# Optimization experiments

Measured on AMD Instinct MI355X. Metric: run time of the kernel, lower is better.

The kernel has to match this reference:

```python
import jax, jax.numpy as jnp
import numpy as np

B, I, H = 65536, 256, 256

def setup_inputs() -> dict:
    key = jax.random.key(0)
    ks = jax.random.split(key, 7)
    stdv = 1.0 / np.sqrt(H)
    u = lambda k, shape: jax.random.uniform(k, shape, jnp.float32, -stdv, stdv)
    return {
        "x":  jax.random.normal(ks[0], (B, I), jnp.float32),
        "h":  jax.random.normal(ks[1], (B, H), jnp.float32),
        "c":  jax.random.normal(ks[2], (B, H), jnp.float32),
        "Wi": u(ks[3], (4, H, I)),   # stacked [W_ii, W_if, W_ig, W_io], torch layout [out,in]
        "Wh": u(ks[4], (4, H, H)),   # stacked [W_hi, W_hf, W_hg, W_ho]
        "bi": u(ks[5], (4, H)),
        "bh": u(ks[6], (4, H)),
    }

def reference(x, h, c, Wi, Wh, bi, bh):
    # Fused version of 8 separate Linears: two batched GEMMs + one elementwise pass.
    # gates[b, k, h] = x @ Wi[k].T + h_prev @ Wh[k].T + bi[k] + bh[k]
    gates = (jnp.einsum('bi,khi->bkh', x, Wi)
             + jnp.einsum('bj,khj->bkh', h, Wh)
             + bi[None] + bh[None])
    i = jax.nn.sigmoid(gates[:, 0])
    f = jax.nn.sigmoid(gates[:, 1])
    g = jnp.tanh(gates[:, 2])
    o = jax.nn.sigmoid(gates[:, 3])
    c_new = f * c + i * g
    h_new = o * jnp.tanh(c_new)
    return (h_new, c_new)
```

## Files before the change

### kernel.cpp

```cpp
#include <hip/hip_runtime.h>
#include <stdint.h>

#define B_DIM 65536
#define HOFF  16777216

typedef __attribute__((ext_vector_type(8))) short short8;
typedef __attribute__((ext_vector_type(8))) unsigned short ushort8_t;
typedef __attribute__((ext_vector_type(4))) float f32x4;

__device__ __forceinline__ unsigned short f2bf(float f) {
  unsigned int u = __builtin_bit_cast(unsigned int, f);
  u += 0x7FFFu + ((u >> 16) & 1u);
  return (unsigned short)(u >> 16);
}
__device__ __forceinline__ float sigf(float x) { return 1.0f / (1.0f + __expf(-x)); }
__device__ __forceinline__ float tanh_fast(float x) {
  float a = fabsf(x);
  float e = __expf(-2.0f * a);
  float t = (1.0f - e) / (1.0f + e);
  return x < 0.0f ? -t : t;
}

typedef const __attribute__((address_space(1))) unsigned int* as1p;
typedef __attribute__((address_space(3))) unsigned int* as3p;
__device__ __forceinline__ void llds16(const unsigned short* g, unsigned short* l) {
  __builtin_amdgcn_global_load_lds((as1p)g, (as3p)l, 16, 0, 0);
}

__global__ void prep_a(const float* __restrict__ x, const float* __restrict__ h,
                       ushort8_t* __restrict__ A8) {
  unsigned o = blockIdx.x * 256u + threadIdx.x;
  unsigned b = o >> 6, c8 = o & 63u;
  const float* src = (c8 < 32u) ? x + (size_t)b * 256u + c8 * 8u
                                : h + (size_t)b * 256u + (c8 - 32u) * 8u;
  float4 v0 = *(const float4*)src;
  float4 v1 = *(const float4*)(src + 4);
  ushort8_t p;
  p[0] = f2bf(v0.x); p[1] = f2bf(v0.y); p[2] = f2bf(v0.z); p[3] = f2bf(v0.w);
  p[4] = f2bf(v1.x); p[5] = f2bf(v1.y); p[6] = f2bf(v1.z); p[7] = f2bf(v1.w);
  A8[o] = p;
}

__global__ void prep_w(const float* __restrict__ Wi, const float* __restrict__ Wh,
                       ushort8_t* __restrict__ W8) {
  unsigned o = blockIdx.x * 256u + threadIdx.x;
  unsigned n = o >> 6, c8 = o & 63u;
  const float* src = (c8 < 32u) ? Wi + (size_t)n * 256u + c8 * 8u
                                : Wh + (size_t)n * 256u + (c8 - 32u) * 8u;
  float4 v0 = *(const float4*)src;
  float4 v1 = *(const float4*)(src + 4);
  ushort8_t p;
  p[0] = f2bf(v0.x); p[1] = f2bf(v0.y); p[2] = f2bf(v0.z); p[3] = f2bf(v0.w);
  p[4] = f2bf(v1.x); p[5] = f2bf(v1.y); p[6] = f2bf(v1.z); p[7] = f2bf(v1.w);
  W8[o] = p;
}

__global__ __launch_bounds__(256, 4) void lstm_gemm(
    const unsigned short* __restrict__ A,
    const unsigned short* __restrict__ W,
    const float* __restrict__ cprev,
    const float* __restrict__ bi, const float* __restrict__ bh,
    float* __restrict__ out) {
  __shared__ unsigned short sA[128 * 32];
  __shared__ unsigned short sB[128 * 32];

  const int t = threadIdx.x;
  const int wid = t >> 6, lane = t & 63;
  const int m = lane & 15, q = lane >> 4;
  const int b0 = (int)(blockIdx.x >> 3) * 128;
  const int h0 = (int)(blockIdx.x & 7) * 32;
  const int R = (wid >> 1) * 64, Cc = (wid & 1) * 64;
  const int hcol = h0 + ((Cc >> 6) << 4) + m;

  const int l4 = lane >> 2;
  const int sg0 = wid * 2, sg1 = wid * 2 + 1;
  const int r0 = sg0 * 16 + l4, r1 = sg1 * 16 + l4;
  const int ck = ((lane & 3) ^ ((l4 >> 1) & 3)) * 8;
  const unsigned aO0 = (unsigned)(b0 + r0) * 512u + (unsigned)ck;
  const unsigned aO1 = (unsigned)(b0 + r1) * 512u + (unsigned)ck;
  const int n0 = (((r0 >> 4) & 3) << 8) + h0 + (r0 & 15) + ((r0 >> 6) << 4);
  const int n1 = (((r1 >> 4) & 3) << 8) + h0 + (r1 & 15) + ((r1 >> 6) << 4);
  const unsigned wO0 = (unsigned)n0 * 512u + (unsigned)ck;
  const unsigned wO1 = (unsigned)n1 * 512u + (unsigned)ck;
  unsigned short* dA0 = &sA[sg0 * 512];
  unsigned short* dA1 = &sA[sg1 * 512];
  unsigned short* dB0 = &sB[sg0 * 512];
  unsigned short* dB1 = &sB[sg1 * 512];

  const int swz = (q ^ ((m >> 1) & 3)) * 8;

  f32x4 acc[4][4];
#pragma unroll
  for (int j = 0; j < 4; ++j) {
    float bv = bi[(j << 8) + hcol] + bh[(j << 8) + hcol];
    f32x4 z = {bv, bv, bv, bv};
#pragma unroll
    for (int i = 0; i < 4; ++i) acc[i][j] = z;
  }

  for (int kt = 0; kt < 16; ++kt) {
    const unsigned k0 = kt * 32u;
    llds16(A + aO0 + k0, dA0);
    llds16(A + aO1 + k0, dA1);
    llds16(W + wO0 + k0, dB0);
    llds16(W + wO1 + k0, dB1);
    __syncthreads();
    short8 av[4], bv[4];
#pragma unroll
    for (int i = 0; i < 4; ++i)
      av[i] = *(const short8*)&sA[(R + i * 16 + m) * 32 + swz];
#pragma unroll
    for (int j = 0; j < 4; ++j)
      bv[j] = *(const short8*)&sB[(Cc + j * 16 + m) * 32 + swz];
#pragma unroll
    for (int i = 0; i < 4; ++i)
#pragma unroll
      for (int j = 0; j < 4; ++j)
        acc[i][j] = __builtin_amdgcn_mfma_f32_16x16x32_bf16(av[i], bv[j], acc[i][j], 0, 0, 0);
    __syncthreads();
  }

  const float* cp = cprev + hcol;
  float* oh = out + hcol;
  float* oc = out + HOFF + hcol;
#pragma unroll
  for (int i = 0; i < 4; ++i) {
    const int br = b0 + R + i * 16 + (q << 2);
    float cv[4];
#pragma unroll
    for (int r = 0; r < 4; ++r) cv[r] = cp[(size_t)(br + r) << 8];
#pragma unroll
    for (int r = 0; r < 4; ++r) {
      float iv = sigf(acc[i][0][r]);
      float fv = sigf(acc[i][1][r]);
      float gv = tanh_fast(acc[i][2][r]);
      float ov = sigf(acc[i][3][r]);
      float cn = fv * cv[r] + iv * gv;
      oh[(size_t)(br + r) << 8] = ov * tanh_fast(cn);
      oc[(size_t)(br + r) << 8] = cn;
    }
  }
}

__global__ void lstm_naive(const float* __restrict__ x, const float* __restrict__ h,
                           const float* __restrict__ c,
                           const float* __restrict__ Wi, const float* __restrict__ Wh,
                           const float* __restrict__ bi, const float* __restrict__ bh,
                           float* __restrict__ out) {
  int gid = blockIdx.x * 256 + threadIdx.x;
  int b = gid >> 8, hh = gid & 255;
  float a0 = bi[hh] + bh[hh];
  float a1 = bi[256 + hh] + bh[256 + hh];
  float a2 = bi[512 + hh] + bh[512 + hh];
  float a3 = bi[768 + hh] + bh[768 + hh];
  const float* xr = x + (size_t)b * 256;
  const float* hr = h + (size_t)b * 256;
  const float* w0 = Wi + (size_t)hh * 256;
  const float* w1 = Wh + (size_t)hh * 256;
  for (int i = 0; i < 256; ++i) {
    float xv = xr[i];
    a0 += xv * w0[i]; a1 += xv * w0[65536 + i];
    a2 += xv * w0[131072 + i]; a3 += xv * w0[196608 + i];
  }
  for (int i = 0; i < 256; ++i) {
    float hv = hr[i];
    a0 += hv * w1[i]; a1 += hv * w1[65536 + i];
    a2 += hv * w1[131072 + i]; a3 += hv * w1[196608 + i];
  }
  float iv = sigf(a0), fv = sigf(a1), gv = tanh_fast(a2), ov = sigf(a3);
  float cn = fv * c[gid] + iv * gv;
  out[gid] = ov * tanh_fast(cn);
  out[HOFF + gid] = cn;
}

extern "C" void kernel_launch(void* const* d_in, const int* in_sizes, int n_in,
                              void* d_out, int out_size, void* d_ws, size_t ws_size,
                              hipStream_t stream) {
  const float* x  = (const float*)d_in[0];
  const float* h  = (const float*)d_in[1];
  const float* c  = (const float*)d_in[2];
  const float* Wi = (const float*)d_in[3];
  const float* Wh = (const float*)d_in[4];
  const float* bi = (const float*)d_in[5];
  const float* bh = (const float*)d_in[6];
  float* out = (float*)d_out;

  const size_t needA = (size_t)B_DIM * 512 * 2;
  const size_t needW = (size_t)1024 * 512 * 2;
  if (ws_size >= needA + needW) {
    ushort8_t* A8 = (ushort8_t*)d_ws;
    ushort8_t* W8 = (ushort8_t*)((char*)d_ws + needA);
    hipLaunchKernelGGL(prep_a, dim3(B_DIM * 64 / 256), dim3(256), 0, stream, x, h, A8);
    hipLaunchKernelGGL(prep_w, dim3(1024 * 64 / 256), dim3(256), 0, stream, Wi, Wh, W8);
    hipLaunchKernelGGL(lstm_gemm, dim3((B_DIM / 128) * 8), dim3(256), 0, stream,
                       (const unsigned short*)A8, (const unsigned short*)W8,
                       c, bi, bh, out);
  } else {
    hipLaunchKernelGGL(lstm_naive, dim3(B_DIM), dim3(256), 0, stream,
                       x, h, c, Wi, Wh, bi, bh, out);
  }
}
```

Baseline: 417.3 us.

## Fuse activation bf16 conversion into GEMM with pipelined loads and LDS-staged epilogue

Result: slower. 448.7 us (+7.5%).

```diff
diff --git a/kernel.cpp b/kernel.cpp
--- a/kernel.cpp
+++ b/kernel.cpp
@@ -8,11 +8,16 @@
 typedef __attribute__((ext_vector_type(8))) unsigned short ushort8_t;
 typedef __attribute__((ext_vector_type(4))) float f32x4;
 
-__device__ __forceinline__ unsigned short f2bf(float f) {
-  unsigned int u = __builtin_bit_cast(unsigned int, f);
+__device__ __forceinline__ unsigned f2bf_u(float f) {
+  unsigned u = __builtin_bit_cast(unsigned, f);
   u += 0x7FFFu + ((u >> 16) & 1u);
-  return (unsigned short)(u >> 16);
-}
+  return u >> 16;
+}
+__device__ __forceinline__ unsigned pack2(float lo, float hi) {
+  return f2bf_u(lo) | (f2bf_u(hi) << 16);
+}
+__device__ __forceinline__ unsigned short f2bf(float f) { return (unsigned short)f2bf_u(f); }
+
 __device__ __forceinline__ float sigf(float x) { return 1.0f / (1.0f + __expf(-x)); }
 __device__ __forceinline__ float tanh_fast(float x) {
   float a = fabsf(x);
@@ -27,19 +32,8 @@
   __builtin_amdgcn_global_load_lds((as1p)g, (as3p)l, 16, 0, 0);
 }
 
-__global__ void prep_a(const float* __restrict__ x, const float* __restrict__ h,
-                       ushort8_t* __restrict__ A8) {
-  unsigned o = blockIdx.x * 256u + threadIdx.x;
-  unsigned b = o >> 6, c8 = o & 63u;
-  const float* src = (c8 < 32u) ? x + (size_t)b * 256u + c8 * 8u
-                                : h + (size_t)b * 256u + (c8 - 32u) * 8u;
-  float4 v0 = *(const float4*)src;
-  float4 v1 = *(const float4*)(src + 4);
-  ushort8_t p;
-  p[0] = f2bf(v0.x); p[1] = f2bf(v0.y); p[2] = f2bf(v0.z); p[3] = f2bf(v0.w);
-  p[4] = f2bf(v1.x); p[5] = f2bf(v1.y); p[6] = f2bf(v1.z); p[7] = f2bf(v1.w);
-  A8[o] = p;
-}
+#define SYNC_LGKM() asm volatile("s_waitcnt lgkmcnt(0)\n\ts_barrier" ::: "memory")
+#define WAVE_LDS_FENCE() asm volatile("s_waitcnt lgkmcnt(0)" ::: "memory")
 
 __global__ void prep_w(const float* __restrict__ Wi, const float* __restrict__ Wh,
                        ushort8_t* __restrict__ W8) {
@@ -55,90 +49,125 @@
   W8[o] = p;
 }
 
-__global__ __launch_bounds__(256, 4) void lstm_gemm(
-    const unsigned short* __restrict__ A,
+__global__ __launch_bounds__(256, 3) void lstm_fused(
+    const float* __restrict__ X, const float* __restrict__ Hs,
     const unsigned short* __restrict__ W,
     const float* __restrict__ cprev,
     const float* __restrict__ bi, const float* __restrict__ bh,
     float* __restrict__ out) {
-  __shared__ unsigned short sA[128 * 32];
-  __shared__ unsigned short sB[128 * 32];
+  __shared__ union {
+    struct { unsigned short A[128 * 32]; unsigned short B[2][128 * 32]; } s;
+    float ep[4 * 1152];
+  } sm;
 
   const int t = threadIdx.x;
   const int wid = t >> 6, lane = t & 63;
   const int m = lane & 15, q = lane >> 4;
   const int b0 = (int)(blockIdx.x >> 3) * 128;
   const int h0 = (int)(blockIdx.x & 7) * 32;
-  const int R = (wid >> 1) * 64, Cc = (wid & 1) * 64;
-  const int hcol = h0 + ((Cc >> 6) << 4) + m;
+  const int R = wid * 32;
 
   const int l4 = lane >> 2;
-  const int sg0 = wid * 2, sg1 = wid * 2 + 1;
-  const int r0 = sg0 * 16 + l4, r1 = sg1 * 16 + l4;
-  const int ck = ((lane & 3) ^ ((l4 >> 1) & 3)) * 8;
-  const unsigned aO0 = (unsigned)(b0 + r0) * 512u + (unsigned)ck;
-  const unsigned aO1 = (unsigned)(b0 + r1) * 512u + (unsigned)ck;
-  const int n0 = (((r0 >> 4) & 3) << 8) + h0 + (r0 & 15) + ((r0 >> 6) << 4);
-  const int n1 = (((r1 >> 4) & 3) << 8) + h0 + (r1 & 15) + ((r1 >> 6) << 4);
-  const unsigned wO0 = (unsigned)n0 * 512u + (unsigned)ck;
-  const unsigned wO1 = (unsigned)n1 * 512u + (unsigned)ck;
-  unsigned short* dA0 = &sA[sg0 * 512];
-  unsigned short* dA1 = &sA[sg1 * 512];
-  unsigned short* dB0 = &sB[sg0 * 512];
-  unsigned short* dB1 = &sB[sg1 * 512];
-
-  const int swz = (q ^ ((m >> 1) & 3)) * 8;
-
-  f32x4 acc[4][4];
-#pragma unroll
-  for (int j = 0; j < 4; ++j) {
-    float bv = bi[(j << 8) + hcol] + bh[(j << 8) + hcol];
-    f32x4 z = {bv, bv, bv, bv};
-#pragma unroll
-    for (int i = 0; i < 4; ++i) acc[i][j] = z;
-  }
-
+  const int sg0 = wid * 2, sg1 = sg0 + 1;
+  const int c0 = sg0 * 16 + l4, c1 = sg1 * 16 + l4;
+  const int ckb = ((lane & 3) ^ ((l4 >> 1) & 3)) * 8;
+  const int n0 = (((c0 >> 4) & 3) << 8) + h0 + (c0 & 15) + ((c0 >> 6) << 4);
+  const int n1 = (((c1 >> 4) & 3) << 8) + h0 + (c1 & 15) + ((c1 >> 6) << 4);
+  const unsigned wO0 = (unsigned)n0 * 512u + (unsigned)ckb;
+  const unsigned wO1 = (unsigned)n1 * 512u + (unsigned)ckb;
+
+  const int ar = t >> 1, hf = t & 1;
+  const unsigned aoff = (unsigned)(b0 + ar) * 256u + (unsigned)hf * 16u;
+  const int slot0 = (2 * hf) ^ ((ar >> 1) & 3), slot1 = slot0 ^ 1;
+  uint4* dA0 = (uint4*)&sm.s.A[ar * 32 + slot0 * 8];
+  uint4* dA1 = (uint4*)&sm.s.A[ar * 32 + slot1 * 8];
+
+  const int swzb = (q ^ ((m >> 1) & 3)) * 8;
+  const unsigned short* aRd = &sm.s.A[(R + m) * 32 + swzb];
+  const int bRdOff = m * 32 + swzb;
+
+  f32x4 acc[2][8];
+#pragma unroll
+  for (int jj = 0; jj < 8; ++jj) {
+    int g = jj & 3, hcol = h0 + ((jj >> 2) << 4) + m;
+    float bvv = bi[(g << 8) + hcol] + bh[(g << 8) + hcol];
+    f32x4 z = {bvv, bvv, bvv, bvv};
+    acc[0][jj] = z; acc[1][jj] = z;
+  }
+
+  float4 a0, a1, a2, a3;
+  { const float* p = X + aoff;
+    a0 = *(const float4*)p;       a1 = *(const float4*)(p + 4);
+    a2 = *(const float4*)(p + 8); a3 = *(const float4*)(p + 12); }
+  llds16(W + wO0, &sm.s.B[0][sg0 * 512]);
+  llds16(W + wO1, &sm.s.B[0][sg1 * 512]);
+
+#pragma unroll 2
   for (int kt = 0; kt < 16; ++kt) {
-    const unsigned k0 = kt * 32u;
-    llds16(A + aO0 + k0, dA0);
-    llds16(A + aO1 + k0, dA1);
-    llds16(W + wO0 + k0, dB0);
-    llds16(W + wO1 + k0, dB1);
+    const int cur = kt & 1, nxt = cur ^ 1;
+    uint4 u0, u1;
+    u0.x = pack2(a0.x, a0.y); u0.y = pack2(a0.z, a0.w);
+    u0.z = pack2(a1.x, a1.y); u0.w = pack2(a1.z, a1.w);
+    u1.x = pack2(a2.x, a2.y); u1.y = pack2(a2.z, a2.w);
+    u1.z = pack2(a3.x, a3.y); u1.w = pack2(a3.z, a3.w);
+    *dA0 = u0; *dA1 = u1;
     __syncthreads();
-    short8 av[4], bv[4];
-#pragma unroll
-    for (int i = 0; i < 4; ++i)
-      av[i] = *(const short8*)&sA[(R + i * 16 + m) * 32 + swz];
-#pragma unroll
-    for (int j = 0; j < 4; ++j)
-      bv[j] = *(const short8*)&sB[(Cc + j * 16 + m) * 32 + swz];
-#pragma unroll
-    for (int i = 0; i < 4; ++i)
-#pragma unroll
-      for (int j = 0; j < 4; ++j)
-        acc[i][j] = __builtin_amdgcn_mfma_f32_16x16x32_bf16(av[i], bv[j], acc[i][j], 0, 0, 0);
-    __syncthreads();
-  }
-
-  const float* cp = cprev + hcol;
-  float* oh = out + hcol;
-  float* oc = out + HOFF + hcol;
-#pragma unroll
-  for (int i = 0; i < 4; ++i) {
-    const int br = b0 + R + i * 16 + (q << 2);
-    float cv[4];
-#pragma unroll
-    for (int r = 0; r < 4; ++r) cv[r] = cp[(size_t)(br + r) << 8];
-#pragma unroll
-    for (int r = 0; r < 4; ++r) {
-      float iv = sigf(acc[i][0][r]);
-      float fv = sigf(acc[i][1][r]);
-      float gv = tanh_fast(acc[i][2][r]);
-      float ov = sigf(acc[i][3][r]);
-      float cn = fv * cv[r] + iv * gv;
-      oh[(size_t)(br + r) << 8] = ov * tanh_fast(cn);
-      oc[(size_t)(br + r) << 8] = cn;
+    if (kt < 15) {
+      llds16(W + wO0 + (unsigned)(kt + 1) * 32u, &sm.s.B[nxt][sg0 * 512]);
+      llds16(W + wO1 + (unsigned)(kt + 1) * 32u, &sm.s.B[nxt][sg1 * 512]);
     }
+    short8 av[2], bv[8];
+    av[0] = *(const short8*)aRd;
+    av[1] = *(const short8*)(aRd + 16 * 32);
+#pragma unroll
+    for (int jj = 0; jj < 8; ++jj)
+      bv[jj] = *(const short8*)&sm.s.B[cur][jj * 512 + bRdOff];
+    if (kt < 15) {
+      const float* src = ((kt + 1) < 8) ? X : Hs;
+      const float* p = src + aoff + ((unsigned)(kt + 1) & 7u) * 32u;
+      a0 = *(const float4*)p;       a1 = *(const float4*)(p + 4);
+      a2 = *(const float4*)(p + 8); a3 = *(const float4*)(p + 12);
+    }
+    SYNC_LGKM();
+#pragma unroll
+    for (int i = 0; i < 2; ++i)
+#pragma unroll
+      for (int jj = 0; jj < 8; ++jj)
+        acc[i][jj] = __builtin_amdgcn_mfma_f32_16x16x32_bf16(av[i], bv[jj], acc[i][jj], 0, 0, 0);
+  }
+
+  float* EB = sm.ep + wid * 1152;
+  const int ROWB = b0 + R;
+#pragma unroll
+  for (int i = 0; i < 2; ++i) {
+#pragma unroll
+    for (int ch = 0; ch < 2; ++ch)
+#pragma unroll
+      for (int r = 0; r < 4; ++r) {
+        int row = ROWB + i * 16 + q * 4 + r;
+        float cv = cprev[(size_t)row * 256 + h0 + ch * 16 + m];
+        float iv = sigf(acc[i][ch * 4 + 0][r]);
+        float fv = sigf(acc[i][ch * 4 + 1][r]);
+        float gv = tanh_fast(acc[i][ch * 4 + 2][r]);
+        float ov = sigf(acc[i][ch * 4 + 3][r]);
+        float cn = fv * cv + iv * gv;
+        float hn = ov * tanh_fast(cn);
+        int lrow = q * 4 + r, col = ch * 16 + m;
+        EB[lrow * 36 + col] = hn;
+        EB[576 + lrow * 36 + col] = cn;
+      }
+    WAVE_LDS_FENCE();
+    int lr = lane & 15, cb = (lane >> 4) * 8;
+    float4 hv0 = *(const float4*)&EB[lr * 36 + cb];
+    float4 hv1 = *(const float4*)&EB[lr * 36 + cb + 4];
+    float4 cv0 = *(const float4*)&EB[576 + lr * 36 + cb];
+    float4 cv1 = *(const float4*)&EB[576 + lr * 36 + cb + 4];
+    size_t gro = (size_t)(ROWB + i * 16 + lr) * 256 + h0 + cb;
+    *(float4*)&out[gro] = hv0;
+    *(float4*)&out[gro + 4] = hv1;
+    *(float4*)&out[HOFF + gro] = cv0;
+    *(float4*)&out[HOFF + gro + 4] = cv1;
+    if (i == 0) WAVE_LDS_FENCE();
   }
 }
 
@@ -185,16 +214,12 @@
   const float* bh = (const float*)d_in[6];
   float* out = (float*)d_out;
 
-  const size_t needA = (size_t)B_DIM * 512 * 2;
   const size_t needW = (size_t)1024 * 512 * 2;
-  if (ws_size >= needA + needW) {
-    ushort8_t* A8 = (ushort8_t*)d_ws;
-    ushort8_t* W8 = (ushort8_t*)((char*)d_ws + needA);
-    hipLaunchKernelGGL(prep_a, dim3(B_DIM * 64 / 256), dim3(256), 0, stream, x, h, A8);
+  if (ws_size >= needW) {
+    ushort8_t* W8 = (ushort8_t*)d_ws;
     hipLaunchKernelGGL(prep_w, dim3(1024 * 64 / 256), dim3(256), 0, stream, Wi, Wh, W8);
-    hipLaunchKernelGGL(lstm_gemm, dim3((B_DIM / 128) * 8), dim3(256), 0, stream,
-                       (const unsigned short*)A8, (const unsigned short*)W8,
-                       c, bi, bh, out);
+    hipLaunchKernelGGL(lstm_fused, dim3((B_DIM / 128) * 8), dim3(256), 0, stream,
+                       x, h, (const unsigned short*)W8, c, bi, bh, out);
   } else {
     hipLaunchKernelGGL(lstm_naive, dim3(B_DIM), dim3(256), 0, stream,
                        x, h, c, Wi, Wh, bi, bh, out);
```
